# Kernel optimization log

Measured on AMD Instinct MI355X. Metric: run time of the kernel, lower is better.

## Reference

```python
import math
import jax, jax.numpy as jnp
import numpy as np

B, L, D_MODEL = 2, 2048, 1024
N_HEAD, HEAD_DIM = 16, 64
ATT_SCALE = 1.0  # divisor is sqrt(head_dim ** attention_scale)


def setup_inputs() -> dict:
    key = jax.random.key(0)
    ks = jax.random.split(key, 6)
    HD = N_HEAD * HEAD_DIM
    # Xavier-uniform style init for projection weights (stored as [in, out])
    def xavier(k, fan_in, fan_out):
        lim = math.sqrt(6.0 / (fan_in + fan_out))
        return jax.random.uniform(k, (fan_in, fan_out), jnp.float32, -lim, lim)
    return {
        "x":  jax.random.normal(ks[0], (B, L, D_MODEL), jnp.float32),
        "Wq": xavier(ks[1], D_MODEL, HD), "bq": jnp.zeros((HD,), jnp.float32),
        "Wk": xavier(ks[2], D_MODEL, HD), "bk": jnp.zeros((HD,), jnp.float32),
        "Wv": xavier(ks[3], D_MODEL, HD), "bv": jnp.zeros((HD,), jnp.float32),
        "Wo": xavier(ks[4], HD, D_MODEL),
        "bo": jax.random.uniform(ks[5], (D_MODEL,), jnp.float32, -1.0 / math.sqrt(HD), 1.0 / math.sqrt(HD)),
    }


def reference(x, Wq, bq, Wk, bk, Wv, bv, Wo, bo):
    b, l, _ = x.shape
    # QKV projections -> [B, L, H, Dh]
    q = (x @ Wq + bq).reshape(b, l, N_HEAD, HEAD_DIM)
    k = (x @ Wk + bk).reshape(b, l, N_HEAD, HEAD_DIM)
    v = (x @ Wv + bv).reshape(b, l, N_HEAD, HEAD_DIM)
    scale = 1.0 / math.sqrt(HEAD_DIM ** ATT_SCALE)
    # Unnormalized (no softmax) attention: (Q K^T / sqrt(Dh)) V
    scores = jnp.einsum("blhd,bmhd->bhlm", q, k) * scale  # [B,H,L,L]
    attn = jnp.einsum("bhlm,bmhd->blhd", scores, v)        # [B,L,H,Dh]
    out = attn.reshape(b, l, N_HEAD * HEAD_DIM) @ Wo + bo  # dispatcher
    return out
```

## Files before the change

### kernel.cpp

```cpp
#include <hip/hip_runtime.h>
#include <stdint.h>

#define B_ 2
#define L_ 2048
#define DM 1024
#define NH 16
#define DH 64
#define M_ (B_*L_)

typedef short short8 __attribute__((ext_vector_type(8)));
typedef float f32x4 __attribute__((ext_vector_type(4)));

__device__ __forceinline__ unsigned short f2b(float f) {
    union { float f; unsigned int u; } v; v.f = f;
    unsigned int u = v.u;
    return (unsigned short)((u + 0x7fffu + ((u >> 16) & 1u)) >> 16);
}

__device__ __forceinline__ void gld_lds16(const void* g, void* l) {
    __builtin_amdgcn_global_load_lds(
        (const __attribute__((address_space(1))) void*)g,
        (__attribute__((address_space(3))) void*)l, 16, 0, 0);
}

__global__ __launch_bounds__(256)
void setup_kernel(const float* __restrict__ x,
                  const float* __restrict__ Wq, const float* __restrict__ Wk,
                  const float* __restrict__ Wv, const float* __restrict__ Wo,
                  const float* __restrict__ bq, const float* __restrict__ bk,
                  const float* __restrict__ bv,
                  unsigned short* __restrict__ xb, unsigned short* __restrict__ WqkvT,
                  unsigned short* __restrict__ WoT, float* __restrict__ biasq,
                  float* __restrict__ KtV)
{
    __shared__ float tile[32][33];
    const int bid = blockIdx.x;
    const int t = threadIdx.x;

    if (bid < 2048) {
        int i = (bid * 256 + t) * 8;
        float4 a0 = *(const float4*)(x + i);
        float4 a1 = *(const float4*)(x + i + 4);
        uint4 p;
        p.x = (unsigned)f2b(a0.x) | ((unsigned)f2b(a0.y) << 16);
        p.y = (unsigned)f2b(a0.z) | ((unsigned)f2b(a0.w) << 16);
        p.z = (unsigned)f2b(a1.x) | ((unsigned)f2b(a1.y) << 16);
        p.w = (unsigned)f2b(a1.z) | ((unsigned)f2b(a1.w) << 16);
        *(uint4*)(xb + i) = p;
    } else if (bid < 2048 + 4096) {
        int wb = bid - 2048;
        int wi = wb >> 10;
        int tid = wb & 1023;
        const float* W = (wi == 0) ? Wq : (wi == 1) ? Wk : (wi == 2) ? Wv : Wo;
        float s = (wi == 1) ? 0.125f : 1.0f;
        int n0 = (tid & 31) * 32, k0 = (tid >> 5) * 32;
        int r = t >> 3, c4 = (t & 7) << 2;
        float4 v = *(const float4*)(W + (size_t)(k0 + r) * DM + n0 + c4);
        tile[r][c4+0] = v.x; tile[r][c4+1] = v.y; tile[r][c4+2] = v.z; tile[r][c4+3] = v.w;
        __syncthreads();
        uint2 o;
        o.x = (unsigned)f2b(tile[c4+0][r]*s) | ((unsigned)f2b(tile[c4+1][r]*s) << 16);
        o.y = (unsigned)f2b(tile[c4+2][r]*s) | ((unsigned)f2b(tile[c4+3][r]*s) << 16);
        int f = n0 + r;
        size_t drow;
        unsigned short* dst;
        if (wi == 0)      { dst = WqkvT; drow = f; }
        else if (wi == 1) { dst = WqkvT; drow = 1024 + (f >> 6) * 128 + (f & 63); }
        else if (wi == 2) { dst = WqkvT; drow = 1024 + (f >> 6) * 128 + 64 + (f & 63); }
        else              { dst = WoT;   drow = f; }
        *(uint2*)(dst + drow * DM + k0 + c4) = o;
    } else if (bid < 2048 + 4096 + 12) {
        int n = (bid - 6144) * 256 + t;
        float v;
        if (n < 1024) v = bq[n];
        else {
            int kv = (n - 1024) >> 7, r = (n - 1024) & 127;
            v = (r < 64) ? 0.125f * bk[kv * 64 + r] : bv[kv * 64 + (r - 64)];
        }
        biasq[n] = v;
    } else {
        int i = ((bid - 6156) * 256 + t) * 4;
        float4 z; z.x = z.y = z.z = z.w = 0.f;
        *(float4*)(KtV + i) = z;
    }
}

__global__ __launch_bounds__(512, 2)
void qkv_fused_kernel(const unsigned short* __restrict__ A,
                      const unsigned short* __restrict__ Bt,
                      const float* __restrict__ biasq,
                      unsigned short* __restrict__ Qb,
                      float* __restrict__ KtV)
{
    __shared__ __align__(16) char smem[131072];

    const int bid = blockIdx.x;
    const int mt = bid & 15;
    const int nt = bid >> 4;
    const int m0 = mt * 256, n0 = nt * 256;

    const int t = threadIdx.x;
    const int w = t >> 6, lane = t & 63;
    const int quad = lane >> 4, l16 = lane & 15;
    const int wr = w >> 2, wc = w & 3;

    f32x4 acc[8][4];
    #pragma unroll
    for (int i = 0; i < 8; i++)
        #pragma unroll
        for (int j = 0; j < 4; j++)
            #pragma unroll
            for (int r = 0; r < 4; r++) acc[i][j][r] = 0.f;

    const int c0 = t, c1 = 512 + t;
    const int row0 = c0 >> 2, g0 = (c0 & 3) ^ ((row0 >> 1) & 3);
    const int row1 = c1 >> 2, g1 = (c1 & 3) ^ ((row1 >> 1) & 3);

    auto STAGE_A = [&](int buf, int kk) {
        gld_lds16(A + (size_t)(m0 + row0) * DM + kk + g0 * 8,
                  smem + buf * 32768 + w * 1024);
        gld_lds16(A + (size_t)(m0 + row1) * DM + kk + g1 * 8,
                  smem + buf * 32768 + 8192 + w * 1024);
    };
    auto STAGE_B = [&](int buf, int kk) {
        gld_lds16(Bt + (size_t)(n0 + row0) * DM + kk + g0 * 8,
                  smem + buf * 32768 + 16384 + w * 1024);
        gld_lds16(Bt + (size_t)(n0 + row1) * DM + kk + g1 * 8,
                  smem + buf * 32768 + 16384 + 8192 + w * 1024);
    };

    STAGE_A(0, 0);  STAGE_B(0, 0);
    STAGE_A(1, 32); STAGE_B(1, 32);

    int cur = 0, st = 2;
    short8 bf[4], af[4];

    for (int T = 0; T < 31; T++) {
        asm volatile("s_waitcnt vmcnt(4)" ::: "memory");
        __builtin_amdgcn_sched_barrier(0);
        __builtin_amdgcn_s_barrier();
        __builtin_amdgcn_sched_barrier(0);

        const char* Ab = smem + cur * 32768;
        const char* Bb = Ab + 16384;

        if (T < 30) STAGE_A(st, (T + 2) * 32);
        #pragma unroll
        for (int j = 0; j < 4; j++) {
            int bn = wc * 64 + j * 16 + l16;
            bf[j] = *(const short8*)(Bb + bn * 64 + ((quad ^ ((bn >> 1) & 3)) << 4));
        }
        #pragma unroll
        for (int i = 0; i < 4; i++) {
            int am = wr * 128 + i * 16 + l16;
            af[i] = *(const short8*)(Ab + am * 64 + ((quad ^ ((am >> 1) & 3)) << 4));
        }
        __builtin_amdgcn_s_setprio(1);
        #pragma unroll
        for (int i = 0; i < 4; i++)
            #pragma unroll
            for (int j = 0; j < 4; j++)
                acc[i][j] = __builtin_amdgcn_mfma_f32_16x16x32_bf16(af[i], bf[j], acc[i][j], 0, 0, 0);
        __builtin_amdgcn_s_setprio(0);

        if (T < 30) STAGE_B(st, (T + 2) * 32);
        #pragma unroll
        for (int i = 0; i < 4; i++) {
            int am = wr * 128 + (i + 4) * 16 + l16;
            af[i] = *(const short8*)(Ab + am * 64 + ((quad ^ ((am >> 1) & 3)) << 4));
        }
        __builtin_amdgcn_s_setprio(1);
        #pragma unroll
        for (int i = 0; i < 4; i++)
            #pragma unroll
            for (int j = 0; j < 4; j++)
                acc[i + 4][j] = __builtin_amdgcn_mfma_f32_16x16x32_bf16(af[i], bf[j], acc[i + 4][j], 0, 0, 0);
        __builtin_amdgcn_s_setprio(0);

        cur = (cur == 2) ? 0 : cur + 1;
        st  = (st  == 2) ? 0 : st  + 1;
    }

    asm volatile("s_waitcnt vmcnt(0)" ::: "memory");
    __builtin_amdgcn_sched_barrier(0);
    __builtin_amdgcn_s_barrier();
    __builtin_amdgcn_sched_barrier(0);
    {
        const char* Ab = smem + cur * 32768;
        const char* Bb = Ab + 16384;
        #pragma unroll
        for (int j = 0; j < 4; j++) {
            int bn = wc * 64 + j * 16 + l16;
            bf[j] = *(const short8*)(Bb + bn * 64 + ((quad ^ ((bn >> 1) & 3)) << 4));
        }
        #pragma unroll
        for (int i = 0; i < 4; i++) {
            int am = wr * 128 + i * 16 + l16;
            af[i] = *(const short8*)(Ab + am * 64 + ((quad ^ ((am >> 1) & 3)) << 4));
        }
        #pragma unroll
        for (int i = 0; i < 4; i++)
            #pragma unroll
            for (int j = 0; j < 4; j++)
                acc[i][j] = __builtin_amdgcn_mfma_f32_16x16x32_bf16(af[i], bf[j], acc[i][j], 0, 0, 0);
        #pragma unroll
        for (int i = 0; i < 4; i++) {
            int am = wr * 128 + (i + 4) * 16 + l16;
            af[i] = *(const short8*)(Ab + am * 64 + ((quad ^ ((am >> 1) & 3)) << 4));
        }
        #pragma unroll
        for (int i = 0; i < 4; i++)
            #pragma unroll
            for (int j = 0; j < 4; j++)
                acc[i + 4][j] = __builtin_amdgcn_mfma_f32_16x16x32_bf16(af[i], bf[j], acc[i + 4][j], 0, 0, 0);
    }

    #pragma unroll
    for (int j = 0; j < 4; j++) {
        float bv = biasq[n0 + wc * 64 + j * 16 + l16];
        #pragma unroll
        for (int i = 0; i < 8; i++)
            #pragma unroll
            for (int r = 0; r < 4; r++) acc[i][j][r] += bv;
    }

    if (nt < 4) {
        #pragma unroll
        for (int j = 0; j < 4; j++) {
            int col = n0 + wc * 64 + j * 16 + l16;
            #pragma unroll
            for (int i = 0; i < 8; i++) {
                #pragma unroll
                for (int r = 0; r < 4; r++) {
                    int row = m0 + wr * 128 + i * 16 + quad * 4 + r;
                    Qb[(size_t)row * DM + col] = f2b(acc[i][j][r]);
                }
            }
        }
        return;
    }

    __builtin_amdgcn_sched_barrier(0);
    __builtin_amdgcn_s_barrier();

    #pragma unroll
    for (int j = 0; j < 4; j++) {
        int c = wc * 64 + j * 16 + l16;
        int cs = (c & 7) << 4;
        #pragma unroll
        for (int i = 0; i < 8; i++) {
            int l0 = wr * 128 + i * 16 + quad * 4;
            uint2 o;
            o.x = (unsigned)f2b(acc[i][j][0]) | ((unsigned)f2b(acc[i][j][1]) << 16);
            o.y = (unsigned)f2b(acc[i][j][2]) | ((unsigned)f2b(acc[i][j][3]) << 16);
            *(uint2*)(smem + c * 512 + ((l0 * 2) ^ cs)) = o;
        }
    }
    __builtin_amdgcn_sched_barrier(0);
    __builtin_amdgcn_s_barrier();

    const int hh = w >> 2;
    const int s  = w & 3;
    const int bb = mt >> 3;
    const int h  = (nt - 4) * 2 + hh;

    f32x4 kacc[4];
    #pragma unroll
    for (int j = 0; j < 4; j++)
        #pragma unroll
        for (int r = 0; r < 4; r++) kacc[j][r] = 0.f;

    #pragma unroll
    for (int ks = 0; ks < 8; ks++) {
        int ca = hh * 128 + s * 16 + l16;
        short8 afk = *(const short8*)(smem + ca * 512 + ((ks * 64 + quad * 16) ^ ((ca & 7) << 4)));
        #pragma unroll
        for (int j = 0; j < 4; j++) {
            int cb = hh * 128 + 64 + j * 16 + l16;
            short8 bfk = *(const short8*)(smem + cb * 512 + ((ks * 64 + quad * 16) ^ ((cb & 7) << 4)));
            kacc[j] = __builtin_amdgcn_mfma_f32_16x16x32_bf16(afk, bfk, kacc[j], 0, 0, 0);
        }
    }

    float* dst = KtV + (size_t)(bb * NH + h) * 64 * 64;
    #pragma unroll
    for (int j = 0; j < 4; j++) {
        int col = j * 16 + l16;
        #pragma unroll
        for (int r = 0; r < 4; r++) {
            int row = s * 16 + quad * 4 + r;
            atomicAdd(dst + row * 64 + col, kacc[j][r]);
        }
    }
}

__global__ __launch_bounds__(256)
void zmat_kernel(const unsigned short* __restrict__ WoT, const float* __restrict__ KtV,
                 unsigned short* __restrict__ ZT)
{
    __shared__ __align__(16) unsigned short Asl[64][72];
    __shared__ __align__(16) unsigned short Bsl[64][72];

    const int bh = blockIdx.x, nt0 = blockIdx.y;
    const int b = bh >> 4, h = bh & 15;
    const int t = threadIdx.x;
    const int wave = t >> 6, lane = t & 63;
    const int quad = lane >> 4, l16 = lane & 15;
    const int n0 = nt0 * 64;
    const int row = t >> 2, c0 = (t & 3) << 4;

    const unsigned short* ap = WoT + (size_t)(n0 + row) * DM + h * DH + c0;
    *(uint4*)&Asl[row][c0]     = *(const uint4*)ap;
    *(uint4*)&Asl[row][c0 + 8] = *(const uint4*)(ap + 8);

    const float* kp = KtV + ((size_t)bh * 64 + row) * 64 + c0;
    #pragma unroll
    for (int j = 0; j < 16; j++) Bsl[row][c0 + j] = f2b(kp[j]);
    __syncthreads();

    f32x4 acc[4];
    #pragma unroll
    for (int i = 0; i < 4; i++)
        #pragma unroll
        for (int r = 0; r < 4; r++) acc[i][r] = 0.f;

    #pragma unroll
    for (int ks = 0; ks < 2; ks++) {
        short8 af = *(const short8*)&Asl[wave * 16 + l16][ks * 32 + quad * 8];
        #pragma unroll
        for (int nt = 0; nt < 4; nt++) {
            short8 bfr = *(const short8*)&Bsl[nt * 16 + l16][ks * 32 + quad * 8];
            acc[nt] = __builtin_amdgcn_mfma_f32_16x16x32_bf16(af, bfr, acc[nt], 0, 0, 0);
        }
    }

    unsigned short* zb = ZT + (size_t)b * 1024 * 1024 + (size_t)h * DH;
    #pragma unroll
    for (int nt = 0; nt < 4; nt++) {
        int col = nt * 16 + l16;
        #pragma unroll
        for (int r = 0; r < 4; r++) {
            int zr = n0 + wave * 16 + quad * 4 + r;
            zb[(size_t)zr * 1024 + col] = f2b(acc[nt][r]);
        }
    }
}

__global__ __launch_bounds__(256)
void out_gemm_kernel(const unsigned short* __restrict__ A,
                     const unsigned short* __restrict__ Bt,
                     const float* __restrict__ bias,
                     float* __restrict__ C)
{
    __shared__ __align__(16) char smem[73728];

    const int bid = blockIdx.x;
    const int xcd = bid & 7, local = bid >> 3;
    const int mt = xcd * 4 + (local & 3);
    const int nt = local >> 2;
    const int m0 = mt * 128, n0 = nt * 64;

    const int t = threadIdx.x;
    const int w = t >> 6, lane = t & 63;
    const int quad = lane >> 4, l16 = lane & 15;

    const unsigned short* Btb = Bt + (size_t)(m0 >> 11) * 1024 * 1024;

    f32x4 acc[2][4];
    #pragma unroll
    for (int i = 0; i < 2; i++)
        #pragma unroll
        for (int j = 0; j < 4; j++)
            #pragma unroll
            for (int r = 0; r < 4; r++) acc[i][j][r] = 0.f;

    auto STAGE = [&](int buf, int kk) {
        #pragma unroll
        for (int p = 0; p < 4; p++) {
            int c = p * 256 + t;
            int row = c >> 3, slot = c & 7;
            int g = slot ^ ((row >> 1) & 7);
            gld_lds16(A + (size_t)(m0 + row) * DM + kk + g * 8,
                      smem + buf * 24576 + p * 4096 + w * 1024);
        }
        #pragma unroll
        for (int p = 0; p < 2; p++) {
            int c = p * 256 + t;
            int row = c >> 3, slot = c & 7;
            int g = slot ^ ((row >> 1) & 7);
            gld_lds16(Btb + (size_t)(n0 + row) * DM + kk + g * 8,
                      smem + buf * 24576 + 16384 + p * 4096 + w * 1024);
        }
    };
    auto COMPUTE = [&](int buf) {
        const char* Asb = smem + buf * 24576;
        const char* Bsb = Asb + 16384;
        #pragma unroll
        for (int ks = 0; ks < 2; ks++) {
            int kc = ks * 4 + quad;
            short8 afr[2], bfr[4];
            #pragma unroll
            for (int i = 0; i < 2; i++) {
                int am = w * 32 + i * 16 + l16;
                afr[i] = *(const short8*)(Asb + am * 128 + ((kc ^ ((am >> 1) & 7)) << 4));
            }
            #pragma unroll
            for (int j = 0; j < 4; j++) {
                int bn = j * 16 + l16;
                bfr[j] = *(const short8*)(Bsb + bn * 128 + ((kc ^ ((bn >> 1) & 7)) << 4));
            }
            __builtin_amdgcn_s_setprio(1);
            #pragma unroll
            for (int i = 0; i < 2; i++)
                #pragma unroll
                for (int j = 0; j < 4; j++)
                    acc[i][j] = __builtin_amdgcn_mfma_f32_16x16x32_bf16(afr[i], bfr[j], acc[i][j], 0, 0, 0);
            __builtin_amdgcn_s_setprio(0);
        }
    };

    STAGE(0, 0);
    STAGE(1, 64);

    int cur = 0, st = 2;
    for (int T = 0; T < 15; T++) {
        asm volatile("s_waitcnt vmcnt(6)" ::: "memory");
        __builtin_amdgcn_sched_barrier(0);
        __builtin_amdgcn_s_barrier();
        __builtin_amdgcn_sched_barrier(0);

        if (T < 14) STAGE(st, (T + 2) * 64);
        COMPUTE(cur);

        cur = (cur == 2) ? 0 : cur + 1;
        st  = (st  == 2) ? 0 : st  + 1;
    }
    asm volatile("s_waitcnt vmcnt(0)" ::: "memory");
    __builtin_amdgcn_sched_barrier(0);
    __builtin_amdgcn_s_barrier();
    __builtin_amdgcn_sched_barrier(0);
    COMPUTE(cur);

    #pragma unroll
    for (int j = 0; j < 4; j++) {
        int col = n0 + j * 16 + l16;
        float bv = bias[col];
        #pragma unroll
        for (int i = 0; i < 2; i++) {
            #pragma unroll
            for (int r = 0; r < 4; r++) {
                int row = m0 + w * 32 + i * 16 + quad * 4 + r;
                C[(size_t)row * DM + col] = acc[i][j][r] + bv;
            }
        }
    }
}


extern "C" void kernel_launch(void* const* d_in, const int* in_sizes, int n_in,
                              void* d_out, int out_size, void* d_ws, size_t ws_size,
                              hipStream_t stream)
{
    const float* x  = (const float*)d_in[0];
    const float* Wq = (const float*)d_in[1];
    const float* bq = (const float*)d_in[2];
    const float* Wk = (const float*)d_in[3];
    const float* bk = (const float*)d_in[4];
    const float* Wv = (const float*)d_in[5];
    const float* bv = (const float*)d_in[6];
    const float* Wo = (const float*)d_in[7];
    const float* bo = (const float*)d_in[8];

    char* ws = (char*)d_ws;
    unsigned short* xb    = (unsigned short*)(ws);
    unsigned short* WqkvT = (unsigned short*)(ws + (size_t)8  * 1024 * 1024);
    unsigned short* WoT   = (unsigned short*)(ws + (size_t)14 * 1024 * 1024);
    float*          biasq = (float*)         (ws + (size_t)16 * 1024 * 1024);
    unsigned short* Qb    = (unsigned short*)(ws + (size_t)17 * 1024 * 1024);
    unsigned short* ZT    = (unsigned short*)(ws + (size_t)25 * 1024 * 1024);
    float*          KtV   = (float*)         (ws + (size_t)29 * 1024 * 1024);

    setup_kernel<<<6284, 256, 0, stream>>>(x, Wq, Wk, Wv, Wo, bq, bk, bv,
                                           xb, WqkvT, WoT, biasq, KtV);

    qkv_fused_kernel<<<192, 512, 0, stream>>>(xb, WqkvT, biasq, Qb, KtV);

    zmat_kernel<<<dim3(B_ * NH, 16), 256, 0, stream>>>(WoT, KtV, ZT);

    out_gemm_kernel<<<512, 256, 0, stream>>>(Qb, ZT, bo, (float*)d_out);
}
```

Before: 138.3 us.

## Halve QKV GEMM N-tile to 128 and double block count with XCD-aware mapping

The fused QKV GEMM now uses 256x128 output tiles instead of 256x256, which doubles the grid from 192 to 384 blocks so the GPU's compute units are better filled. Block IDs are remapped so each XCD works on adjacent M tiles, to improve L2 reuse. Per-block LDS drops to 72 KB and the launch bound allows more resident blocks, while the K^T V epilogue is reworked so each block covers one head and waves split the reduction. In exchange, each block reuses data less per byte loaded and the atomic adds into KtV double.

```diff
diff --git a/kernel.cpp b/kernel.cpp
--- a/kernel.cpp
+++ b/kernel.cpp
@@ -85,154 +85,109 @@
     }
 }
 
-__global__ __launch_bounds__(512, 2)
+__global__ __launch_bounds__(512, 4)
 void qkv_fused_kernel(const unsigned short* __restrict__ A,
                       const unsigned short* __restrict__ Bt,
                       const float* __restrict__ biasq,
                       unsigned short* __restrict__ Qb,
                       float* __restrict__ KtV)
 {
-    __shared__ __align__(16) char smem[131072];
+    __shared__ __align__(16) char smem[73728];
 
     const int bid = blockIdx.x;
-    const int mt = bid & 15;
-    const int nt = bid >> 4;
-    const int m0 = mt * 256, n0 = nt * 256;
+    const int xcd = bid & 7, local = bid >> 3;
+    const int mt = xcd * 2 + (local & 1);
+    const int nt = local >> 1;
+    const int m0 = mt * 256, n0 = nt * 128;
 
     const int t = threadIdx.x;
     const int w = t >> 6, lane = t & 63;
     const int quad = lane >> 4, l16 = lane & 15;
-    const int wr = w >> 2, wc = w & 3;
-
-    f32x4 acc[8][4];
-    #pragma unroll
-    for (int i = 0; i < 8; i++)
+    const int wr = w >> 1, wc = w & 1;
+
+    f32x4 acc[4][4];
+    #pragma unroll
+    for (int i = 0; i < 4; i++)
         #pragma unroll
         for (int j = 0; j < 4; j++)
             #pragma unroll
             for (int r = 0; r < 4; r++) acc[i][j][r] = 0.f;
 
-    const int c0 = t, c1 = 512 + t;
-    const int row0 = c0 >> 2, g0 = (c0 & 3) ^ ((row0 >> 1) & 3);
-    const int row1 = c1 >> 2, g1 = (c1 & 3) ^ ((row1 >> 1) & 3);
-
-    auto STAGE_A = [&](int buf, int kk) {
-        gld_lds16(A + (size_t)(m0 + row0) * DM + kk + g0 * 8,
-                  smem + buf * 32768 + w * 1024);
-        gld_lds16(A + (size_t)(m0 + row1) * DM + kk + g1 * 8,
-                  smem + buf * 32768 + 8192 + w * 1024);
+    const int rA0 = t >> 2,        gA0 = (t & 3) ^ ((rA0 >> 1) & 3);
+    const int rA1 = 128 + (t >> 2), gA1 = (t & 3) ^ ((rA1 >> 1) & 3);
+    const int rB  = t >> 2,        gB  = (t & 3) ^ ((rB  >> 1) & 3);
+
+    auto STAGE = [&](int buf, int kk) {
+        gld_lds16(A + (size_t)(m0 + rA0) * DM + kk + gA0 * 8,
+                  smem + buf * 24576 + w * 1024);
+        gld_lds16(A + (size_t)(m0 + rA1) * DM + kk + gA1 * 8,
+                  smem + buf * 24576 + 8192 + w * 1024);
+        gld_lds16(Bt + (size_t)(n0 + rB) * DM + kk + gB * 8,
+                  smem + buf * 24576 + 16384 + w * 1024);
     };
-    auto STAGE_B = [&](int buf, int kk) {
-        gld_lds16(Bt + (size_t)(n0 + row0) * DM + kk + g0 * 8,
-                  smem + buf * 32768 + 16384 + w * 1024);
-        gld_lds16(Bt + (size_t)(n0 + row1) * DM + kk + g1 * 8,
-                  smem + buf * 32768 + 16384 + 8192 + w * 1024);
+    auto COMPUTE = [&](int buf) {
+        const char* Ab = smem + buf * 24576;
+        const char* Bb = Ab + 16384;
+        short8 af[4], bf[4];
+        #pragma unroll
+        for (int j = 0; j < 4; j++) {
+            int bn = wc * 64 + j * 16 + l16;
+            bf[j] = *(const short8*)(Bb + bn * 64 + ((quad ^ ((bn >> 1) & 3)) << 4));
+        }
+        #pragma unroll
+        for (int i = 0; i < 4; i++) {
+            int am = wr * 64 + i * 16 + l16;
+            af[i] = *(const short8*)(Ab + am * 64 + ((quad ^ ((am >> 1) & 3)) << 4));
+        }
+        __builtin_amdgcn_s_setprio(1);
+        #pragma unroll
+        for (int i = 0; i < 4; i++)
+            #pragma unroll
+            for (int j = 0; j < 4; j++)
+                acc[i][j] = __builtin_amdgcn_mfma_f32_16x16x32_bf16(af[i], bf[j], acc[i][j], 0, 0, 0);
+        __builtin_amdgcn_s_setprio(0);
     };
 
-    STAGE_A(0, 0);  STAGE_B(0, 0);
-    STAGE_A(1, 32); STAGE_B(1, 32);
+    STAGE(0, 0);
+    STAGE(1, 32);
 
     int cur = 0, st = 2;
-    short8 bf[4], af[4];
-
     for (int T = 0; T < 31; T++) {
-        asm volatile("s_waitcnt vmcnt(4)" ::: "memory");
+        asm volatile("s_waitcnt vmcnt(3)" ::: "memory");
         __builtin_amdgcn_sched_barrier(0);
         __builtin_amdgcn_s_barrier();
         __builtin_amdgcn_sched_barrier(0);
 
-        const char* Ab = smem + cur * 32768;
-        const char* Bb = Ab + 16384;
-
-        if (T < 30) STAGE_A(st, (T + 2) * 32);
-        #pragma unroll
-        for (int j = 0; j < 4; j++) {
-            int bn = wc * 64 + j * 16 + l16;
-            bf[j] = *(const short8*)(Bb + bn * 64 + ((quad ^ ((bn >> 1) & 3)) << 4));
-        }
-        #pragma unroll
-        for (int i = 0; i < 4; i++) {
-            int am = wr * 128 + i * 16 + l16;
-            af[i] = *(const short8*)(Ab + am * 64 + ((quad ^ ((am >> 1) & 3)) << 4));
-        }
-        __builtin_amdgcn_s_setprio(1);
-        #pragma unroll
-        for (int i = 0; i < 4; i++)
-            #pragma unroll
-            for (int j = 0; j < 4; j++)
-                acc[i][j] = __builtin_amdgcn_mfma_f32_16x16x32_bf16(af[i], bf[j], acc[i][j], 0, 0, 0);
-        __builtin_amdgcn_s_setprio(0);
-
-        if (T < 30) STAGE_B(st, (T + 2) * 32);
-        #pragma unroll
-        for (int i = 0; i < 4; i++) {
-            int am = wr * 128 + (i + 4) * 16 + l16;
-            af[i] = *(const short8*)(Ab + am * 64 + ((quad ^ ((am >> 1) & 3)) << 4));
-        }
-        __builtin_amdgcn_s_setprio(1);
-        #pragma unroll
-        for (int i = 0; i < 4; i++)
-            #pragma unroll
-            for (int j = 0; j < 4; j++)
-                acc[i + 4][j] = __builtin_amdgcn_mfma_f32_16x16x32_bf16(af[i], bf[j], acc[i + 4][j], 0, 0, 0);
-        __builtin_amdgcn_s_setprio(0);
+        if (T < 30) STAGE(st, (T + 2) * 32);
+        COMPUTE(cur);
 
         cur = (cur == 2) ? 0 : cur + 1;
         st  = (st  == 2) ? 0 : st  + 1;
     }
-
     asm volatile("s_waitcnt vmcnt(0)" ::: "memory");
     __builtin_amdgcn_sched_barrier(0);
     __builtin_amdgcn_s_barrier();
     __builtin_amdgcn_sched_barrier(0);
-    {
-        const char* Ab = smem + cur * 32768;
-        const char* Bb = Ab + 16384;
-        #pragma unroll
-        for (int j = 0; j < 4; j++) {
-            int bn = wc * 64 + j * 16 + l16;
-            bf[j] = *(const short8*)(Bb + bn * 64 + ((quad ^ ((bn >> 1) & 3)) << 4));
-        }
-        #pragma unroll
-        for (int i = 0; i < 4; i++) {
-            int am = wr * 128 + i * 16 + l16;
-            af[i] = *(const short8*)(Ab + am * 64 + ((quad ^ ((am >> 1) & 3)) << 4));
-        }
-        #pragma unroll
-        for (int i = 0; i < 4; i++)
-            #pragma unroll
-            for (int j = 0; j < 4; j++)
-                acc[i][j] = __builtin_amdgcn_mfma_f32_16x16x32_bf16(af[i], bf[j], acc[i][j], 0, 0, 0);
-        #pragma unroll
-        for (int i = 0; i < 4; i++) {
-            int am = wr * 128 + (i + 4) * 16 + l16;
-            af[i] = *(const short8*)(Ab + am * 64 + ((quad ^ ((am >> 1) & 3)) << 4));
-        }
-        #pragma unroll
-        for (int i = 0; i < 4; i++)
-            #pragma unroll
-            for (int j = 0; j < 4; j++)
-                acc[i + 4][j] = __builtin_amdgcn_mfma_f32_16x16x32_bf16(af[i], bf[j], acc[i + 4][j], 0, 0, 0);
-    }
+    COMPUTE(cur);
 
     #pragma unroll
     for (int j = 0; j < 4; j++) {
         float bv = biasq[n0 + wc * 64 + j * 16 + l16];
         #pragma unroll
-        for (int i = 0; i < 8; i++)
+        for (int i = 0; i < 4; i++)
             #pragma unroll
             for (int r = 0; r < 4; r++) acc[i][j][r] += bv;
     }
 
-    if (nt < 4) {
+    if (nt < 8) {
         #pragma unroll
         for (int j = 0; j < 4; j++) {
             int col = n0 + wc * 64 + j * 16 + l16;
             #pragma unroll
-            for (int i = 0; i < 8; i++) {
+            for (int i = 0; i < 4; i++) {
                 #pragma unroll
                 for (int r = 0; r < 4; r++) {
-                    int row = m0 + wr * 128 + i * 16 + quad * 4 + r;
+                    int row = m0 + wr * 64 + i * 16 + quad * 4 + r;
                     Qb[(size_t)row * DM + col] = f2b(acc[i][j][r]);
                 }
             }
@@ -248,8 +203,8 @@
         int c = wc * 64 + j * 16 + l16;
         int cs = (c & 7) << 4;
         #pragma unroll
-        for (int i = 0; i < 8; i++) {
-            int l0 = wr * 128 + i * 16 + quad * 4;
+        for (int i = 0; i < 4; i++) {
+            int l0 = wr * 64 + i * 16 + quad * 4;
             uint2 o;
             o.x = (unsigned)f2b(acc[i][j][0]) | ((unsigned)f2b(acc[i][j][1]) << 16);
             o.y = (unsigned)f2b(acc[i][j][2]) | ((unsigned)f2b(acc[i][j][3]) << 16);
@@ -259,10 +214,10 @@
     __builtin_amdgcn_sched_barrier(0);
     __builtin_amdgcn_s_barrier();
 
-    const int hh = w >> 2;
     const int s  = w & 3;
+    const int lh = w >> 2;
     const int bb = mt >> 3;
-    const int h  = (nt - 4) * 2 + hh;
+    const int h  = nt - 8;
 
     f32x4 kacc[4];
     #pragma unroll
@@ -271,12 +226,13 @@
         for (int r = 0; r < 4; r++) kacc[j][r] = 0.f;
 
     #pragma unroll
-    for (int ks = 0; ks < 8; ks++) {
-        int ca = hh * 128 + s * 16 + l16;
+    for (int kq = 0; kq < 4; kq++) {
+        int ks = lh * 4 + kq;
+        int ca = s * 16 + l16;
         short8 afk = *(const short8*)(smem + ca * 512 + ((ks * 64 + quad * 16) ^ ((ca & 7) << 4)));
         #pragma unroll
         for (int j = 0; j < 4; j++) {
-            int cb = hh * 128 + 64 + j * 16 + l16;
+            int cb = 64 + j * 16 + l16;
             short8 bfk = *(const short8*)(smem + cb * 512 + ((ks * 64 + quad * 16) ^ ((cb & 7) << 4)));
             kacc[j] = __builtin_amdgcn_mfma_f32_16x16x32_bf16(afk, bfk, kacc[j], 0, 0, 0);
         }
@@ -483,7 +439,7 @@
     setup_kernel<<<6284, 256, 0, stream>>>(x, Wq, Wk, Wv, Wo, bq, bk, bv,
                                            xb, WqkvT, WoT, biasq, KtV);
 
-    qkv_fused_kernel<<<192, 512, 0, stream>>>(xb, WqkvT, biasq, Qb, KtV);
+    qkv_fused_kernel<<<384, 512, 0, stream>>>(xb, WqkvT, biasq, Qb, KtV);
 
     zmat_kernel<<<dim3(B_ * NH, 16), 256, 0, stream>>>(WoT, KtV, ZT);
 
```

New measurement: 142.7 us. 3.2% more time.
